# Performance work log

Hardware: AMD Instinct MI355X
Metric: run time of the kernel (lower is better)

Reference implementation:

```python
import jax, jax.numpy as jnp
import numpy as np

N_USERS = 60000
N_ITEMS = 40000
N_NODES = N_USERS + N_ITEMS  # 100000
N_EDGES = 3_200_000
EMB_DIM = 64
N_LAYERS = 3
S_TEMP = 1.0  # config['s_temp']
EPS = 1e-16   # torch_geometric.utils.softmax denominator eps


def segment_softmax(logits, seg, num_segments):
    # numerically stable scatter-softmax (PyG softmax semantics)
    m = jax.ops.segment_max(logits, seg, num_segments=num_segments)
    m = jnp.where(jnp.isfinite(m), m, 0.0)  # empty segments -> -inf guard
    e = jnp.exp(logits - m[seg])
    s = jax.ops.segment_sum(e, seg, num_segments=num_segments)
    return e / (s[seg] + EPS)


def setup_inputs() -> dict:
    key = jax.random.key(0)
    k1, k2, k3 = jax.random.split(key, 3)
    # nn.Embedding weight, init normal(std=0.1) for non-NGCF models
    emb = jax.random.normal(k1, (N_NODES, EMB_DIM), dtype=jnp.float32) * 0.1
    edge_index = jax.random.randint(k2, (2, N_EDGES), 0, N_NODES, dtype=jnp.int32)
    edge_attrs = jax.random.normal(k3, (N_EDGES,), dtype=jnp.float32)
    return {"emb": emb, "edge_index": edge_index, "edge_attrs": edge_attrs}


def reference(emb, edge_index, edge_attrs):
    from_, to_ = edge_index[0], edge_index[1]
    logits = edge_attrs / S_TEMP
    incoming = segment_softmax(logits, to_, N_NODES)
    outgoing = segment_softmax(logits, from_, N_NODES)
    norm = jnp.sqrt(incoming * outgoing)  # abl_study == 0 branch

    embs = [emb]
    cur = emb
    for _ in range(N_LAYERS):
        # message: norm * x_j ; aggregate: scatter-add at to_
        msg = norm[:, None] * cur[from_]           # [E, D]
        cur = jax.ops.segment_sum(msg, to_, num_segments=N_NODES)  # [N, D]
        embs.append(cur)

    out = jnp.mean(jnp.stack(embs, axis=0), axis=0)  # lightGCN-style layer mean
    return (emb, out)
```

## Files before the change

### kernel.cpp

```cpp
#include <hip/hip_runtime.h>
#include <math.h>
#include <hip/hip_fp16.h>

#define N_NODES 100000
#define N_EDGES 3200000
#define EPS 1e-16f
#define BSH 8
#define BN 256
#define NBK 391
#define PTT 512
#define PE2 8
#define PTILE (PTT * PE2)
#define GR (PTILE / 16)
#define PBLOCKS ((N_EDGES + PTILE - 1) / PTILE)
#define CAP 9216u
#define FSPLIT 50000u

typedef float    f4v __attribute__((ext_vector_type(4)));
typedef float    f2v __attribute__((ext_vector_type(2)));

static __device__ __forceinline__ float4 nt_load_f4(const float4* p) {
    f4v v = __builtin_nontemporal_load((const f4v*)p);
    return make_float4(v.x, v.y, v.z, v.w);
}

static __device__ __forceinline__ unsigned short f_to_bf(float f) {
    unsigned u = __float_as_uint(f);
    unsigned r = (u + 0x7FFFu + ((u >> 16) & 1u)) >> 16;
    return (unsigned short)r;
}
static __device__ __forceinline__ float slot_w(unsigned s) {
    return __half2float(__ushort_as_half((unsigned short)(s >> 17)));
}
static __device__ __forceinline__ void fma8_fp8(float w, uint2 r, float* a) {
    f2v v0 = __builtin_amdgcn_cvt_pk_f32_fp8((int)r.x, false);
    f2v v1 = __builtin_amdgcn_cvt_pk_f32_fp8((int)r.x, true);
    f2v v2 = __builtin_amdgcn_cvt_pk_f32_fp8((int)r.y, false);
    f2v v3 = __builtin_amdgcn_cvt_pk_f32_fp8((int)r.y, true);
    a[0] = fmaf(w, v0.x, a[0]); a[1] = fmaf(w, v0.y, a[1]);
    a[2] = fmaf(w, v1.x, a[2]); a[3] = fmaf(w, v1.y, a[3]);
    a[4] = fmaf(w, v2.x, a[4]); a[5] = fmaf(w, v2.y, a[5]);
    a[6] = fmaf(w, v3.x, a[6]); a[7] = fmaf(w, v3.y, a[7]);
}
static __device__ __forceinline__ uint4 pack8(const float* a) {
    uint4 o;
    o.x = (unsigned)f_to_bf(a[0]) | ((unsigned)f_to_bf(a[1]) << 16);
    o.y = (unsigned)f_to_bf(a[2]) | ((unsigned)f_to_bf(a[3]) << 16);
    o.z = (unsigned)f_to_bf(a[4]) | ((unsigned)f_to_bf(a[5]) << 16);
    o.w = (unsigned)f_to_bf(a[6]) | ((unsigned)f_to_bf(a[7]) << 16);
    return o;
}
static __device__ __forceinline__ uint2 pack8_fp8(const float* a) {
    int w0 = __builtin_amdgcn_cvt_pk_fp8_f32(a[0], a[1], 0, false);
    w0 = __builtin_amdgcn_cvt_pk_fp8_f32(a[2], a[3], w0, true);
    int w1 = __builtin_amdgcn_cvt_pk_fp8_f32(a[4], a[5], 0, false);
    w1 = __builtin_amdgcn_cvt_pk_fp8_f32(a[6], a[7], w1, true);
    return make_uint2((unsigned)w0, (unsigned)w1);
}
static __device__ __forceinline__ float bfu_to_f(unsigned u, int hi) {
    return __uint_as_float(hi ? (u & 0xFFFF0000u) : (u << 16));
}

__global__ __launch_bounds__(PTT) void partition(
        const int* __restrict__ ei, const float* __restrict__ attr,
        unsigned* __restrict__ pos_t, unsigned* __restrict__ pos_f,
        uint2* __restrict__ bt, unsigned* __restrict__ bf,
        const float4* __restrict__ emb4, uint2* __restrict__ emb_f8) {
    __shared__ unsigned ht[NBK], hf[NBK];
    __shared__ unsigned hbt[NBK + 1], hbf[NBK + 1];
    __shared__ unsigned dlt[NBK], dlf[NBK];
    __shared__ unsigned short lutT[GR], lutF[GR];
    __shared__ unsigned wsum[8];
    __shared__ unsigned sbtx[PTILE], sbty[PTILE];
    __shared__ unsigned sbf[PTILE];
    const int tid = threadIdx.x;
    const int lane = tid & 63, wid = tid >> 6;
    for (int i = tid; i < NBK; i += PTT) { ht[i] = 0; hf[i] = 0; }
    __syncthreads();
    const int tile = blockIdx.x * PTILE;
    const int tcount = (tile + PTILE < N_EDGES) ? PTILE : (N_EDGES - tile);
    unsigned fv[PE2], tv[PE2];
    float xv[PE2];
    #pragma unroll
    for (int k = 0; k < PE2; ++k) {
        int e = tile + k * PTT + tid;
        if (e < N_EDGES) {
            fv[k] = (unsigned)__builtin_nontemporal_load(&ei[e]);
            tv[k] = (unsigned)__builtin_nontemporal_load(&ei[N_EDGES + e]);
            xv[k] = __expf(__builtin_nontemporal_load(&attr[e]));
            atomicAdd(&ht[tv[k] >> BSH], 1u);
            atomicAdd(&hf[fv[k] >> BSH], 1u);
        } else {
            tv[k] = 0xFFFFFFFFu;
        }
    }
    __syncthreads();
    unsigned ot = (tid < NBK) ? ht[tid] : 0u;
    unsigned of = (tid < NBK) ? hf[tid] : 0u;
    unsigned own = ot | (of << 16);
    unsigned x = own;
    #pragma unroll
    for (int d = 1; d < 64; d <<= 1) {
        unsigned v = __shfl_up(x, d, 64);
        if (lane >= d) x += v;
    }
    if (lane == 63) wsum[wid] = x;
    __syncthreads();
    unsigned pre = 0;
    for (int w = 0; w < wid; ++w) pre += wsum[w];
    unsigned excl = x + pre - own;
    unsigned et = excl & 0xFFFFu, ef = excl >> 16;
    if (tid < NBK) {
        hbt[tid] = et;
        hbf[tid] = ef;
        unsigned rt = ot ? atomicAdd(&pos_t[tid], ot) : 0u;
        unsigned rf = of ? atomicAdd(&pos_f[tid], of) : 0u;
        dlt[tid] = tid * CAP + rt - et;
        dlf[tid] = tid * CAP + rf - ef;
    }
    if (tid == NBK - 1) { hbt[NBK] = et + ot; hbf[NBK] = ef + of; }
    __syncthreads();
    if (tid < NBK) {
        unsigned b0 = hbt[tid], b1 = hbt[tid + 1];
        for (unsigned g = (b0 + 15u) >> 4; (g << 4) < b1; ++g) lutT[g] = (unsigned short)tid;
        b0 = hbf[tid]; b1 = hbf[tid + 1];
        for (unsigned g = (b0 + 15u) >> 4; (g << 4) < b1; ++g) lutF[g] = (unsigned short)tid;
    }
    for (int i = tid; i < NBK; i += PTT) { ht[i] = hbt[i]; hf[i] = hbf[i]; }
    __syncthreads();
    #pragma unroll
    for (int k = 0; k < PE2; ++k) {
        if (tv[k] != 0xFFFFFFFFu) {
            unsigned p = atomicAdd(&ht[tv[k] >> BSH], 1u);
            sbtx[p] = fv[k] | ((tv[k] & (BN - 1u)) << 17);
            sbty[p] = __float_as_uint(xv[k]);
            unsigned q = atomicAdd(&hf[fv[k] >> BSH], 1u);
            sbf[q] = ((fv[k] & (BN - 1u)) << 16) |
                     (unsigned)__half_as_ushort(__float2half(xv[k]));
        }
    }
    __syncthreads();
    for (int i = tid; i < tcount; i += PTT) {
        unsigned b = lutT[i >> 4];
        while (hbt[b + 1] <= (unsigned)i) ++b;
        unsigned ga = dlt[b] + (unsigned)i;
        if (ga < (b + 1u) * CAP) bt[ga] = make_uint2(sbtx[i], sbty[i]);
    }
    for (int i = tid; i < tcount; i += PTT) {
        unsigned b = lutF[i >> 4];
        while (hbf[b + 1] <= (unsigned)i) ++b;
        unsigned ga = dlf[b] + (unsigned)i;
        if (ga < (b + 1u) * CAP) bf[ga] = sbf[i];
    }
    for (int i = blockIdx.x * PTT + tid; i < N_NODES * 8; i += PBLOCKS * PTT) {
        float4 v0 = nt_load_f4(&emb4[2 * i]);
        float4 v1 = nt_load_f4(&emb4[2 * i + 1]);
        float a[8] = {v0.x, v0.y, v0.z, v0.w, v1.x, v1.y, v1.z, v1.w};
        emb_f8[i] = pack8_fp8(a);
    }
}

__global__ __launch_bounds__(512) void bucket_sum_f(
        const unsigned* __restrict__ pos_f, const unsigned* __restrict__ bf,
        float* __restrict__ s_from_inv) {
    __shared__ float s[BN];
    int b = blockIdx.x, tid = threadIdx.x;
    if (tid < BN) s[tid] = 0.f;
    __syncthreads();
    unsigned fill = pos_f[b]; if (fill > CAP) fill = CAP;
    unsigned lo = b * CAP, hi = lo + fill;
    for (unsigned i = lo + tid; i < hi; i += 512) {
        unsigned u = __builtin_nontemporal_load(&bf[i]);
        atomicAdd(&s[u >> 16], __half2float(__ushort_as_half((unsigned short)(u & 0xFFFFu))));
    }
    __syncthreads();
    if (tid < BN) {
        int node = b * BN + tid;
        if (node < N_NODES) s_from_inv[node] = rsqrtf(s[tid] + EPS);
    }
}

__global__ __launch_bounds__(512) void bucket_csr_t(
        const unsigned* __restrict__ pos_t, const uint2* __restrict__ bt,
        const float* __restrict__ s_from_inv,
        uint2* __restrict__ row2, unsigned* __restrict__ slots) {
    __shared__ unsigned cntL[BN], cntH[BN];
    __shared__ float sto[BN];
    __shared__ float rs[BN];
    __shared__ unsigned curL[BN], curH[BN];
    __shared__ unsigned wsum[8];
    int b = blockIdx.x, tid = threadIdx.x;
    const int lane = tid & 63, wid = tid >> 6;
    if (tid < BN) { cntL[tid] = 0; cntH[tid] = 0; sto[tid] = 0.f; }
    __syncthreads();
    unsigned fill = pos_t[b]; if (fill > CAP) fill = CAP;
    unsigned lo = b * CAP, hi = lo + fill;
    for (unsigned i = lo + tid; i < hi; i += 512) {
        uint2 u = bt[i];
        unsigned tl = u.x >> 17;
        unsigned f = u.x & 0x1FFFFu;
        atomicAdd((f < FSPLIT) ? &cntL[tl] : &cntH[tl], 1u);
        atomicAdd(&sto[tl], __uint_as_float(u.y));
    }
    __syncthreads();
    unsigned ol = (tid < BN) ? cntL[tid] : 0u;
    unsigned oh = (tid < BN) ? cntH[tid] : 0u;
    unsigned own = ol + oh;
    unsigned x = own;
    #pragma unroll
    for (int d = 1; d < 64; d <<= 1) {
        unsigned v = __shfl_up(x, d, 64);
        if (lane >= d) x += v;
    }
    if (lane == 63) wsum[wid] = x;
    __syncthreads();
    unsigned pre = 0;
    for (int w = 0; w < wid; ++w) pre += wsum[w];
    unsigned excl = x + pre - own;
    if (tid < BN) {
        int node = b * BN + tid;
        if (node < N_NODES) row2[node] = make_uint2(lo + excl, lo + excl + own);
        rs[tid] = rsqrtf(sto[tid] + EPS);
        curL[tid] = lo + excl;
        curH[tid] = lo + excl + ol;
    }
    __syncthreads();
    for (unsigned i = lo + tid; i < hi; i += 512) {
        uint2 u = bt[i];
        unsigned tl = u.x >> 17;
        unsigned f = u.x & 0x1FFFFu;
        float w = __uint_as_float(u.y) * rs[tl] * s_from_inv[f];
        unsigned hb = (unsigned)__half_as_ushort(__float2half(w));
        unsigned p = atomicAdd((f < FSPLIT) ? &curL[tl] : &curH[tl], 1u);
        slots[p] = f | (hb << 17);
    }
}

#define GATHER_CORE8(TABLE)                                                       \
    float a[8] = {0, 0, 0, 0, 0, 0, 0, 0};                                        \
    float bacc[8] = {0, 0, 0, 0, 0, 0, 0, 0};                                     \
    unsigned k = beg;                                                             \
    for (; k + 8 <= end; k += 8) {                                                \
        unsigned s0 = slots[k], s1 = slots[k + 1], s2 = slots[k + 2], s3 = slots[k + 3]; \
        unsigned s4 = slots[k + 4], s5 = slots[k + 5], s6 = slots[k + 6], s7 = slots[k + 7]; \
        uint2 r0 = TABLE[(size_t)(s0 & 0x1FFFFu) * 8 + lane];                     \
        uint2 r1 = TABLE[(size_t)(s1 & 0x1FFFFu) * 8 + lane];                     \
        uint2 r2 = TABLE[(size_t)(s2 & 0x1FFFFu) * 8 + lane];                     \
        uint2 r3 = TABLE[(size_t)(s3 & 0x1FFFFu) * 8 + lane];                     \
        uint2 r4 = TABLE[(size_t)(s4 & 0x1FFFFu) * 8 + lane];                     \
        uint2 r5 = TABLE[(size_t)(s5 & 0x1FFFFu) * 8 + lane];                     \
        uint2 r6 = TABLE[(size_t)(s6 & 0x1FFFFu) * 8 + lane];                     \
        uint2 r7 = TABLE[(size_t)(s7 & 0x1FFFFu) * 8 + lane];                     \
        fma8_fp8(slot_w(s0), r0, a);    fma8_fp8(slot_w(s1), r1, bacc);           \
        fma8_fp8(slot_w(s2), r2, a);    fma8_fp8(slot_w(s3), r3, bacc);           \
        fma8_fp8(slot_w(s4), r4, a);    fma8_fp8(slot_w(s5), r5, bacc);           \
        fma8_fp8(slot_w(s6), r6, a);    fma8_fp8(slot_w(s7), r7, bacc);           \
    }                                                                             \
    for (; k < end; ++k) {                                                        \
        unsigned s = slots[k];                                                    \
        uint2 r = TABLE[(size_t)(s & 0x1FFFFu) * 8 + lane];                       \
        fma8_fp8(slot_w(s), r, a);                                                \
    }                                                                             \
    _Pragma("unroll")                                                             \
    for (int j = 0; j < 8; ++j) a[j] += bacc[j];

__global__ void prop1(const uint2* __restrict__ row2, const unsigned* __restrict__ slots,
                      const uint2* __restrict__ emb_f8,
                      uint2* __restrict__ T1f8, uint4* __restrict__ T1bf,
                      const float4* __restrict__ emb4, float4* __restrict__ out_emb4) {
    int node = blockIdx.x * 32 + (threadIdx.x >> 3);
    int lane = threadIdx.x & 7;
    if (node < N_NODES) {
        uint2 rp = row2[node];
        unsigned beg = rp.x, end = rp.y;
        GATHER_CORE8(emb_f8)
        size_t o = (size_t)node * 8 + lane;
        T1bf[o] = pack8(a);
        T1f8[o] = pack8_fp8(a);
    }
    const int total = N_NODES * 16;
    const int stride = ((N_NODES * 8 + 255) / 256) * 256;
    for (int i = blockIdx.x * 256 + threadIdx.x; i < total; i += stride) {
        out_emb4[i] = nt_load_f4(&emb4[i]);
    }
}

__global__ void prop2(const uint2* __restrict__ row2, const unsigned* __restrict__ slots,
                      const uint2* __restrict__ T1f8,
                      uint2* __restrict__ T2f8, uint4* __restrict__ T2bf) {
    int node = blockIdx.x * 32 + (threadIdx.x >> 3);
    int lane = threadIdx.x & 7;
    if (node >= N_NODES) return;
    uint2 rp = row2[node];
    unsigned beg = rp.x, end = rp.y;
    GATHER_CORE8(T1f8)
    size_t o = (size_t)node * 8 + lane;
    T2bf[o] = pack8(a);
    T2f8[o] = pack8_fp8(a);
}

__global__ void prop3(const uint2* __restrict__ row2, const unsigned* __restrict__ slots,
                      const uint2* __restrict__ T2f8,
                      const uint4* __restrict__ T1bf, const uint4* __restrict__ T2bf,
                      const float4* __restrict__ emb4, float4* __restrict__ acc) {
    int node = blockIdx.x * 32 + (threadIdx.x >> 3);
    int lane = threadIdx.x & 7;
    if (node >= N_NODES) return;
    uint2 rp = row2[node];
    unsigned beg = rp.x, end = rp.y;
    GATHER_CORE8(T2f8)
    size_t o = (size_t)node * 8 + lane;
    uint4 t1 = T1bf[o];
    uint4 t2 = T2bf[o];
    unsigned tw1[4] = {t1.x, t1.y, t1.z, t1.w};
    unsigned tw2[4] = {t2.x, t2.y, t2.z, t2.w};
    size_t o4 = (size_t)node * 16 + lane * 2;
    float4 e0 = emb4[o4], e1 = emb4[o4 + 1];
    float e[8] = {e0.x, e0.y, e0.z, e0.w, e1.x, e1.y, e1.z, e1.w};
    float r[8];
    #pragma unroll
    for (int j = 0; j < 8; ++j) {
        float l1v = bfu_to_f(tw1[j >> 1], j & 1);
        float l2v = bfu_to_f(tw2[j >> 1], j & 1);
        r[j] = (e[j] + l1v + l2v + a[j]) * 0.25f;
    }
    acc[o4]     = make_float4(r[0], r[1], r[2], r[3]);
    acc[o4 + 1] = make_float4(r[4], r[5], r[6], r[7]);
}

extern "C" void kernel_launch(void* const* d_in, const int* in_sizes, int n_in,
                              void* d_out, int out_size, void* d_ws, size_t ws_size,
                              hipStream_t stream) {
    const float* emb = (const float*)d_in[0];
    const int* ei = (const int*)d_in[1];
    const float* attr = (const float*)d_in[2];

    float* out_emb = (float*)d_out;
    float* out_acc = out_emb + (size_t)N_NODES * 64;

    char* ws = (char*)d_ws;
    size_t off = 0;
    auto alloc = [&](size_t bytes) -> void* {
        void* p = ws + off;
        off += (bytes + 255) & ~(size_t)255;
        return p;
    };
    unsigned* pos_t   = (unsigned*)alloc((size_t)NBK * 4);
    unsigned* pos_f   = (unsigned*)alloc((size_t)NBK * 4);
    size_t zero_bytes = off;
    uint2*    row2    = (uint2*)   alloc((size_t)N_NODES * 8);
    float* s_from_inv = (float*)   alloc((size_t)N_NODES * 4);
    uint2* bt         = (uint2*)   alloc((size_t)NBK * CAP * 8);
    unsigned* bfa     = (unsigned*)alloc((size_t)NBK * CAP * 4);
    unsigned* slots   = bfa;
    uint2* emb_f8     = (uint2*)   alloc((size_t)N_NODES * 64);
    uint2* T1f8       = (uint2*)   alloc((size_t)N_NODES * 64);
    uint4* T1bf       = (uint4*)   alloc((size_t)N_NODES * 128);
    uint2* T2f8 = (uint2*)bt;
    uint4* T2bf = (uint4*)((char*)bt + (size_t)N_NODES * 64);
    (void)ws_size;

    hipMemsetAsync(d_ws, 0, zero_bytes, stream);

    partition<<<PBLOCKS, PTT, 0, stream>>>(ei, attr, pos_t, pos_f, bt, bfa,
                                           (const float4*)emb, emb_f8);
    bucket_sum_f<<<NBK, 512, 0, stream>>>(pos_f, bfa, s_from_inv);
    bucket_csr_t<<<NBK, 512, 0, stream>>>(pos_t, bt, s_from_inv, row2, slots);

    const int pgrid = (N_NODES * 8 + 255) / 256;
    prop1<<<pgrid, 256, 0, stream>>>(row2, slots, emb_f8, T1f8, T1bf,
                                     (const float4*)emb, (float4*)out_emb);
    prop2<<<pgrid, 256, 0, stream>>>(row2, slots, T1f8, T2f8, T2bf);
    prop3<<<pgrid, 256, 0, stream>>>(row2, slots, T2f8, T1bf, T2bf, (const float4*)emb,
                                     (float4*)out_acc);
}
```

Baseline: 270.6 us.

## Factor per-node softmax normalizers out of edge weights into node-side scaling

```diff
diff --git a/kernel.cpp b/kernel.cpp
--- a/kernel.cpp
+++ b/kernel.cpp
@@ -15,6 +15,7 @@
 #define PBLOCKS ((N_EDGES + PTILE - 1) / PTILE)
 #define CAP 9216u
 #define FSPLIT 50000u
+#define SCALE 8.0f
 
 typedef float    f4v __attribute__((ext_vector_type(4)));
 typedef float    f2v __attribute__((ext_vector_type(2)));
@@ -64,8 +65,7 @@
 __global__ __launch_bounds__(PTT) void partition(
         const int* __restrict__ ei, const float* __restrict__ attr,
         unsigned* __restrict__ pos_t, unsigned* __restrict__ pos_f,
-        uint2* __restrict__ bt, unsigned* __restrict__ bf,
-        const float4* __restrict__ emb4, uint2* __restrict__ emb_f8) {
+        uint2* __restrict__ bt, unsigned* __restrict__ bf) {
     __shared__ unsigned ht[NBK], hf[NBK];
     __shared__ unsigned hbt[NBK + 1], hbf[NBK + 1];
     __shared__ unsigned dlt[NBK], dlf[NBK];
@@ -152,24 +152,19 @@
         unsigned ga = dlf[b] + (unsigned)i;
         if (ga < (b + 1u) * CAP) bf[ga] = sbf[i];
     }
-    for (int i = blockIdx.x * PTT + tid; i < N_NODES * 8; i += PBLOCKS * PTT) {
-        float4 v0 = nt_load_f4(&emb4[2 * i]);
-        float4 v1 = nt_load_f4(&emb4[2 * i + 1]);
-        float a[8] = {v0.x, v0.y, v0.z, v0.w, v1.x, v1.y, v1.z, v1.w};
-        emb_f8[i] = pack8_fp8(a);
-    }
-}
-
-__global__ __launch_bounds__(512) void bucket_sum_f(
+}
+
+__global__ __launch_bounds__(1024) void bucket_sum_f(
         const unsigned* __restrict__ pos_f, const unsigned* __restrict__ bf,
-        float* __restrict__ s_from_inv) {
+        float* __restrict__ s_from_inv,
+        const float4* __restrict__ emb4, uint2* __restrict__ emb_f8) {
     __shared__ float s[BN];
     int b = blockIdx.x, tid = threadIdx.x;
     if (tid < BN) s[tid] = 0.f;
     __syncthreads();
     unsigned fill = pos_f[b]; if (fill > CAP) fill = CAP;
     unsigned lo = b * CAP, hi = lo + fill;
-    for (unsigned i = lo + tid; i < hi; i += 512) {
+    for (unsigned i = lo + tid; i < hi; i += 1024) {
         unsigned u = __builtin_nontemporal_load(&bf[i]);
         atomicAdd(&s[u >> 16], __half2float(__ushort_as_half((unsigned short)(u & 0xFFFFu))));
     }
@@ -178,24 +173,39 @@
         int node = b * BN + tid;
         if (node < N_NODES) s_from_inv[node] = rsqrtf(s[tid] + EPS);
     }
-}
-
-__global__ __launch_bounds__(512) void bucket_csr_t(
+    int nl = tid >> 2;
+    int part = tid & 3;
+    int node = b * BN + nl;
+    if (node < N_NODES) {
+        float rsv = rsqrtf(s[nl] + EPS) * SCALE;
+        size_t rbase = (size_t)node * 16 + part * 4;
+        #pragma unroll
+        for (int c = 0; c < 2; ++c) {
+            float4 v0 = emb4[rbase + c * 2];
+            float4 v1 = emb4[rbase + c * 2 + 1];
+            float a[8] = {v0.x * rsv, v0.y * rsv, v0.z * rsv, v0.w * rsv,
+                          v1.x * rsv, v1.y * rsv, v1.z * rsv, v1.w * rsv};
+            emb_f8[(size_t)node * 8 + part * 2 + c] = pack8_fp8(a);
+        }
+    }
+}
+
+__global__ __launch_bounds__(1024) void bucket_csr_t(
         const unsigned* __restrict__ pos_t, const uint2* __restrict__ bt,
         const float* __restrict__ s_from_inv,
-        uint2* __restrict__ row2, unsigned* __restrict__ slots) {
+        uint2* __restrict__ row2, unsigned* __restrict__ slots,
+        float2* __restrict__ sc2) {
     __shared__ unsigned cntL[BN], cntH[BN];
     __shared__ float sto[BN];
-    __shared__ float rs[BN];
     __shared__ unsigned curL[BN], curH[BN];
-    __shared__ unsigned wsum[8];
+    __shared__ unsigned wsum[16];
     int b = blockIdx.x, tid = threadIdx.x;
     const int lane = tid & 63, wid = tid >> 6;
     if (tid < BN) { cntL[tid] = 0; cntH[tid] = 0; sto[tid] = 0.f; }
     __syncthreads();
     unsigned fill = pos_t[b]; if (fill > CAP) fill = CAP;
     unsigned lo = b * CAP, hi = lo + fill;
-    for (unsigned i = lo + tid; i < hi; i += 512) {
+    for (unsigned i = lo + tid; i < hi; i += 1024) {
         uint2 u = bt[i];
         unsigned tl = u.x >> 17;
         unsigned f = u.x & 0x1FFFFu;
@@ -219,18 +229,20 @@
     unsigned excl = x + pre - own;
     if (tid < BN) {
         int node = b * BN + tid;
-        if (node < N_NODES) row2[node] = make_uint2(lo + excl, lo + excl + own);
-        rs[tid] = rsqrtf(sto[tid] + EPS);
+        if (node < N_NODES) {
+            row2[node] = make_uint2(lo + excl, lo + excl + own);
+            float rt = rsqrtf(sto[tid] + EPS);
+            sc2[node] = make_float2(rt * (1.0f / SCALE), rt * s_from_inv[node]);
+        }
         curL[tid] = lo + excl;
         curH[tid] = lo + excl + ol;
     }
     __syncthreads();
-    for (unsigned i = lo + tid; i < hi; i += 512) {
+    for (unsigned i = lo + tid; i < hi; i += 1024) {
         uint2 u = bt[i];
         unsigned tl = u.x >> 17;
         unsigned f = u.x & 0x1FFFFu;
-        float w = __uint_as_float(u.y) * rs[tl] * s_from_inv[f];
-        unsigned hb = (unsigned)__half_as_ushort(__float2half(w));
+        unsigned hb = (unsigned)__half_as_ushort(__float2half(__uint_as_float(u.y)));
         unsigned p = atomicAdd((f < FSPLIT) ? &curL[tl] : &curH[tl], 1u);
         slots[p] = f | (hb << 17);
     }
@@ -265,7 +277,7 @@
     for (int j = 0; j < 8; ++j) a[j] += bacc[j];
 
 __global__ void prop1(const uint2* __restrict__ row2, const unsigned* __restrict__ slots,
-                      const uint2* __restrict__ emb_f8,
+                      const uint2* __restrict__ emb_f8, const float2* __restrict__ sc2,
                       uint2* __restrict__ T1f8, uint4* __restrict__ T1bf,
                       const float4* __restrict__ emb4, float4* __restrict__ out_emb4) {
     int node = blockIdx.x * 32 + (threadIdx.x >> 3);
@@ -274,9 +286,13 @@
         uint2 rp = row2[node];
         unsigned beg = rp.x, end = rp.y;
         GATHER_CORE8(emb_f8)
+        float2 sc = sc2[node];
+        float own[8], tab[8];
+        #pragma unroll
+        for (int j = 0; j < 8; ++j) { own[j] = a[j] * sc.x; tab[j] = a[j] * sc.y; }
         size_t o = (size_t)node * 8 + lane;
-        T1bf[o] = pack8(a);
-        T1f8[o] = pack8_fp8(a);
+        T1bf[o] = pack8(own);
+        T1f8[o] = pack8_fp8(tab);
     }
     const int total = N_NODES * 16;
     const int stride = ((N_NODES * 8 + 255) / 256) * 256;
@@ -286,7 +302,7 @@
 }
 
 __global__ void prop2(const uint2* __restrict__ row2, const unsigned* __restrict__ slots,
-                      const uint2* __restrict__ T1f8,
+                      const uint2* __restrict__ T1f8, const float2* __restrict__ sc2,
                       uint2* __restrict__ T2f8, uint4* __restrict__ T2bf) {
     int node = blockIdx.x * 32 + (threadIdx.x >> 3);
     int lane = threadIdx.x & 7;
@@ -294,13 +310,17 @@
     uint2 rp = row2[node];
     unsigned beg = rp.x, end = rp.y;
     GATHER_CORE8(T1f8)
+    float2 sc = sc2[node];
+    float own[8], tab[8];
+    #pragma unroll
+    for (int j = 0; j < 8; ++j) { own[j] = a[j] * sc.x; tab[j] = a[j] * sc.y; }
     size_t o = (size_t)node * 8 + lane;
-    T2bf[o] = pack8(a);
-    T2f8[o] = pack8_fp8(a);
+    T2bf[o] = pack8(own);
+    T2f8[o] = pack8_fp8(tab);
 }
 
 __global__ void prop3(const uint2* __restrict__ row2, const unsigned* __restrict__ slots,
-                      const uint2* __restrict__ T2f8,
+                      const uint2* __restrict__ T2f8, const float2* __restrict__ sc2,
                       const uint4* __restrict__ T1bf, const uint4* __restrict__ T2bf,
                       const float4* __restrict__ emb4, float4* __restrict__ acc) {
     int node = blockIdx.x * 32 + (threadIdx.x >> 3);
@@ -309,6 +329,7 @@
     uint2 rp = row2[node];
     unsigned beg = rp.x, end = rp.y;
     GATHER_CORE8(T2f8)
+    float osc = sc2[node].x;
     size_t o = (size_t)node * 8 + lane;
     uint4 t1 = T1bf[o];
     uint4 t2 = T2bf[o];
@@ -322,7 +343,7 @@
     for (int j = 0; j < 8; ++j) {
         float l1v = bfu_to_f(tw1[j >> 1], j & 1);
         float l2v = bfu_to_f(tw2[j >> 1], j & 1);
-        r[j] = (e[j] + l1v + l2v + a[j]) * 0.25f;
+        r[j] = (e[j] + l1v + l2v + a[j] * osc) * 0.25f;
     }
     acc[o4]     = make_float4(r[0], r[1], r[2], r[3]);
     acc[o4 + 1] = make_float4(r[4], r[5], r[6], r[7]);
@@ -350,6 +371,7 @@
     size_t zero_bytes = off;
     uint2*    row2    = (uint2*)   alloc((size_t)N_NODES * 8);
     float* s_from_inv = (float*)   alloc((size_t)N_NODES * 4);
+    float2*   sc2     = (float2*)  alloc((size_t)N_NODES * 8);
     uint2* bt         = (uint2*)   alloc((size_t)NBK * CAP * 8);
     unsigned* bfa     = (unsigned*)alloc((size_t)NBK * CAP * 4);
     unsigned* slots   = bfa;
@@ -362,15 +384,15 @@
 
     hipMemsetAsync(d_ws, 0, zero_bytes, stream);
 
-    partition<<<PBLOCKS, PTT, 0, stream>>>(ei, attr, pos_t, pos_f, bt, bfa,
+    partition<<<PBLOCKS, PTT, 0, stream>>>(ei, attr, pos_t, pos_f, bt, bfa);
+    bucket_sum_f<<<NBK, 1024, 0, stream>>>(pos_f, bfa, s_from_inv,
                                            (const float4*)emb, emb_f8);
-    bucket_sum_f<<<NBK, 512, 0, stream>>>(pos_f, bfa, s_from_inv);
-    bucket_csr_t<<<NBK, 512, 0, stream>>>(pos_t, bt, s_from_inv, row2, slots);
+    bucket_csr_t<<<NBK, 1024, 0, stream>>>(pos_t, bt, s_from_inv, row2, slots, sc2);
 
     const int pgrid = (N_NODES * 8 + 255) / 256;
-    prop1<<<pgrid, 256, 0, stream>>>(row2, slots, emb_f8, T1f8, T1bf,
+    prop1<<<pgrid, 256, 0, stream>>>(row2, slots, emb_f8, sc2, T1f8, T1bf,
                                      (const float4*)emb, (float4*)out_emb);
-    prop2<<<pgrid, 256, 0, stream>>>(row2, slots, T1f8, T2f8, T2bf);
-    prop3<<<pgrid, 256, 0, stream>>>(row2, slots, T2f8, T1bf, T2bf, (const float4*)emb,
-                                     (float4*)out_acc);
-}
+    prop2<<<pgrid, 256, 0, stream>>>(row2, slots, T1f8, sc2, T2f8, T2bf);
+    prop3<<<pgrid, 256, 0, stream>>>(row2, slots, T2f8, sc2, T1bf, T2bf,
+                                     (const float4*)emb, (float4*)out_acc);
+}
```

Measured after the change: 252.4 us. -6.7%, faster.
